# Optimization experiments

Measured on AMD Instinct MI355X. Metric: run time of the kernel, lower is better.

## Reference

```python
import math
import jax, jax.numpy as jnp
import numpy as np

E = 1024   # embed_dim
H = 16     # num_heads
DH = E // H
EPS = 1e-8

def round_ste(x):
    # straight-through round (matches brevitas STE behavior)
    return x + jax.lax.stop_gradient(jnp.round(x) - x)

def _scale(x, qmax):
    # dynamic per-tensor abs-max scale (stand-in for brevitas calibrated scale)
    return jnp.maximum(jnp.max(jnp.abs(x)) / qmax, EPS)

def fq(x, s, qmin, qmax):
    # fake-quantize: quantize to int grid, dequantize back to float
    return jnp.clip(round_ste(x / s), qmin, qmax) * s

def quant_linear(x, W, b):
    # Int8ActPerTensorFloat input, Int8WeightPerTensorFloat (narrow range) weight, Int32Bias
    s_x = _scale(x, 128.0)
    s_w = _scale(W, 127.0)
    xq = fq(x, s_x, -128, 127)
    wq = fq(W, s_w, -127, 127)
    y = xq @ wq.T
    if b is not None:
        s_b = s_x * s_w
        y = y + round_ste(b / s_b) * s_b
    return y

def setup_inputs() -> dict:
    k = jax.random.key(0)
    ks = jax.random.split(k, 7)
    S, B = 1024, 4
    return {
        "query": jax.random.normal(ks[0], (S, B, E), jnp.float32),
        "key": jax.random.normal(ks[1], (S, B, E), jnp.float32),
        "value": jax.random.normal(ks[2], (S, B, E), jnp.float32),
        "in_proj_weight": jax.random.normal(ks[3], (3 * E, E), jnp.float32) * 0.02,
        "in_proj_bias": jax.random.normal(ks[4], (3 * E,), jnp.float32) * 0.02,
        "out_proj_weight": jax.random.normal(ks[5], (E, E), jnp.float32) * 0.02,
        "out_proj_bias": jax.random.normal(ks[6], (E,), jnp.float32) * 0.02,
    }

def reference(query, key, value, in_proj_weight, in_proj_bias, out_proj_weight, out_proj_bias):
    S, B, _ = query.shape
    Wq, Wk, Wv = jnp.split(in_proj_weight, 3, axis=0)
    bq, bk, bv = jnp.split(in_proj_bias, 3)
    # quantized QKV projections (packed in_proj split per-input)
    q = quant_linear(query, Wq, bq)   # (S,B,E)
    k = quant_linear(key, Wk, bk)
    v = quant_linear(value, Wv, bv)

    def to_heads(x):  # (S,B,E) -> (B*H, S, DH)
        return x.reshape(S, B * H, DH).transpose(1, 0, 2)

    q = to_heads(q)
    k = to_heads(k)
    v = to_heads(v)

    # q_scaled quant (int8)
    q = q / math.sqrt(DH)
    q = fq(q, _scale(q, 128.0), -128, 127)
    # k_transposed quant (int8)
    kt = k.transpose(0, 2, 1)  # (B*H, DH, S)
    kt = fq(kt, _scale(kt, 128.0), -128, 127)

    attn = q @ kt                      # (B*H, S, S); softmax_input_quant=None -> identity
    attn = jax.nn.softmax(attn, axis=-1)
    # attn_output_weights quant (uint8)
    s_a = jnp.maximum(jnp.max(attn) / 255.0, EPS)
    attn = jnp.clip(round_ste(attn / s_a), 0, 255) * s_a
    # v quant (int8)
    v = fq(v, _scale(v, 128.0), -128, 127)

    out = attn @ v                     # (B*H, S, DH)
    out = out.transpose(1, 0, 2).reshape(S, B, E)
    out = quant_linear(out, out_proj_weight, out_proj_bias)
    return out
```

## Files before the change

### kernel.cpp

```cpp
#include <hip/hip_runtime.h>
#include <stdint.h>

typedef unsigned short u16;
typedef __attribute__((ext_vector_type(8))) short bf16x8;
typedef __attribute__((ext_vector_type(4))) float f32x4;

#define S_LEN 1024
#define BATCH 4
#define EMB   1024
#define NH    16
#define DHEAD 64
#define BHEAD 64
#define NTOK  4096
#define KDIM  1024
#define NDIM  1024
#define EPSF  1e-8f
#define LOG2E 1.4426950408889634f

#define MFMA16(a,b,c) __builtin_amdgcn_mfma_f32_16x16x32_bf16((a),(b),(c),0,0,0)

#define GLOAD16(g, l) __builtin_amdgcn_global_load_lds( \
    (const __attribute__((address_space(1))) void*)(g), \
    (__attribute__((address_space(3))) void*)(l), 16, 0, 0)

#define EXP2F(x) __builtin_amdgcn_exp2f(x)

__device__ __forceinline__ u16 f2bf(float f){
  return (u16)(__float_as_uint(f) >> 16);
}

__device__ __forceinline__ float wave_max(float v){
#pragma unroll
  for (int off = 32; off > 0; off >>= 1) v = fmaxf(v, __shfl_xor(v, off));
  return v;
}


__global__ void k_zero(float* sc){
  if (threadIdx.x < 16) sc[threadIdx.x] = 0.0f;
}

struct AQDesc { const float* x; u16* y; int n4; int slot; float qdiv; float lo; };
struct AQTable { AQDesc d[7]; };

__global__ __launch_bounds__(256) void k_absmax7(AQTable t, int* __restrict__ sci){
  const int bid = blockIdx.x;
  int seg, b0, nb;
  if (bid < 1536){ seg = bid >> 9; b0 = seg << 9; nb = 512; }
  else { seg = 3 + ((bid - 1536) >> 7); b0 = 1536 + ((seg - 3) << 7); nb = 128; }
  const AQDesc D = t.d[seg];
  float m = 0.0f;
  const float4* x4 = (const float4*)D.x;
  for (int i = (bid - b0)*256 + threadIdx.x; i < D.n4; i += nb*256){
    float4 v = x4[i];
    m = fmaxf(m, fmaxf(fmaxf(fabsf(v.x), fabsf(v.y)), fmaxf(fabsf(v.z), fabsf(v.w))));
  }
  m = wave_max(m);
  __shared__ float red[4];
  int lane = threadIdx.x & 63, w = threadIdx.x >> 6;
  if (lane == 0) red[w] = m;
  __syncthreads();
  if (threadIdx.x == 0){
    float mm = fmaxf(fmaxf(red[0], red[1]), fmaxf(red[2], red[3]));
    atomicMax(sci + D.slot, __float_as_int(mm));
  }
}

__global__ __launch_bounds__(256) void k_quant7(AQTable t, const float* __restrict__ sc){
  const int bid = blockIdx.x;
  int seg, b0, nb;
  if (bid < 1536){ seg = bid >> 9; b0 = seg << 9; nb = 512; }
  else { seg = 3 + ((bid - 1536) >> 7); b0 = 1536 + ((seg - 3) << 7); nb = 128; }
  const AQDesc D = t.d[seg];
  const float s = fmaxf(sc[D.slot] / D.qdiv, EPSF);
  const float lo = D.lo;
  const float4* x4 = (const float4*)D.x;
  for (int i = (bid - b0)*256 + threadIdx.x; i < D.n4; i += nb*256){
    float4 v = x4[i];
    union { u16 o[4]; uint2 u; } ou;
    float tt;
    tt = fminf(fmaxf(rintf(v.x / s), lo), 127.f); ou.o[0] = f2bf(tt);
    tt = fminf(fmaxf(rintf(v.y / s), lo), 127.f); ou.o[1] = f2bf(tt);
    tt = fminf(fmaxf(rintf(v.z / s), lo), 127.f); ou.o[2] = f2bf(tt);
    tt = fminf(fmaxf(rintf(v.w / s), lo), 127.f); ou.o[3] = f2bf(tt);
    ((uint2*)D.y)[i] = ou.u;
  }
}

__global__ __launch_bounds__(256) void k_quant(const float* __restrict__ x,
    u16* __restrict__ y, int n4, const float* __restrict__ sc, int slot){
  const float s = fmaxf(sc[slot] / 128.0f, EPSF);
  const float4* x4 = (const float4*)x;
  for (int i = blockIdx.x*256 + threadIdx.x; i < n4; i += gridDim.x*256){
    float4 v = x4[i];
    union { u16 o[4]; uint2 u; } ou;
    float tt;
    tt = fminf(fmaxf(rintf(v.x / s), -128.f), 127.f); ou.o[0] = f2bf(tt);
    tt = fminf(fmaxf(rintf(v.y / s), -128.f), 127.f); ou.o[1] = f2bf(tt);
    tt = fminf(fmaxf(rintf(v.z / s), -128.f), 127.f); ou.o[2] = f2bf(tt);
    tt = fminf(fmaxf(rintf(v.w / s), -128.f), 127.f); ou.o[3] = f2bf(tt);
    ((uint2*)y)[i] = ou.u;
  }
}

__device__ __forceinline__ void gemm_body(const u16* __restrict__ A,
    const u16* __restrict__ W, const float* __restrict__ bias,
    float* __restrict__ out, float s_b, int rowBase, int colBase,
    int* __restrict__ amax_out, u16 (*As)[64], u16 (*Bs)[64], float* red){
  const int tid = threadIdx.x;
  const int wid = tid >> 6, lane = tid & 63;
  const int wm = wid >> 2, wn = wid & 3;
  const int rr = lane & 15, g = lane >> 4;
  const int srow = wid*8 + (lane >> 3);
  const int sco  = ((lane & 7) ^ (lane >> 3)) << 3;
  const u16* Arow0 = &A[(size_t)(rowBase + srow)*KDIM + sco];
  const u16* Arow1 = &A[(size_t)(rowBase + 64 + srow)*KDIM + sco];
  const u16* Wrow0 = &W[(size_t)(colBase + srow)*KDIM + sco];
  const u16* Wrow1 = &W[(size_t)(colBase + 64 + srow)*KDIM + sco];
  f32x4 c[4][2] = {};
  int aoff[4][2], boff[2][2];
#pragma unroll
  for (int i = 0; i < 4; i++){
    int row = wm*64 + i*16 + rr;
#pragma unroll
    for (int h = 0; h < 2; h++)
      aoff[i][h] = row*64 + (((h*4 + g) ^ (row & 7)) << 3);
  }
#pragma unroll
  for (int j = 0; j < 2; j++){
    int row = wn*32 + j*16 + rr;
#pragma unroll
    for (int h = 0; h < 2; h++)
      boff[j][h] = row*64 + (((h*4 + g) ^ (row & 7)) << 3);
  }
  for (int k0 = 0; k0 < KDIM; k0 += 64){
    __syncthreads();
    GLOAD16(Arow0 + k0, &As[wid*8][0]);
    GLOAD16(Arow1 + k0, &As[64 + wid*8][0]);
    GLOAD16(Wrow0 + k0, &Bs[wid*8][0]);
    GLOAD16(Wrow1 + k0, &Bs[64 + wid*8][0]);
    __syncthreads();
#pragma unroll
    for (int h = 0; h < 2; h++){
      bf16x8 af[4], bfr[2];
#pragma unroll
      for (int i = 0; i < 4; i++) af[i]  = *(const bf16x8*)((const u16*)As + aoff[i][h]);
#pragma unroll
      for (int j = 0; j < 2; j++) bfr[j] = *(const bf16x8*)((const u16*)Bs + boff[j][h]);
#pragma unroll
      for (int i = 0; i < 4; i++)
#pragma unroll
        for (int j = 0; j < 2; j++)
          c[i][j] = MFMA16(af[i], bfr[j], c[i][j]);
    }
  }
  float lmax = 0.0f;
  const int r0 = (lane >> 4) * 4, ccol = lane & 15;
#pragma unroll
  for (int j = 0; j < 2; j++){
    int col = colBase + wn*32 + j*16 + ccol;
    float rb = rintf(bias[col] / s_b);
#pragma unroll
    for (int i = 0; i < 4; i++){
      int rowb = rowBase + wm*64 + i*16 + r0;
#pragma unroll
      for (int rI = 0; rI < 4; rI++){
        float y = s_b * (c[i][j][rI] + rb);
        out[(size_t)(rowb + rI)*NDIM + col] = y;
        lmax = fmaxf(lmax, fabsf(y));
      }
    }
  }
  lmax = wave_max(lmax);
  if (lane == 0) red[wid] = lmax;
  __syncthreads();
  if (tid == 0){
    float mm = red[0];
#pragma unroll
    for (int i2 = 1; i2 < 8; i2++) mm = fmaxf(mm, red[i2]);
    atomicMax(amax_out, __float_as_int(mm));
  }
}

__global__ __launch_bounds__(512) void k_gemm3(const u16* __restrict__ Xall,
    const u16* __restrict__ Wall, const float* __restrict__ ball,
    float* __restrict__ Yall, const float* __restrict__ sc, int* __restrict__ sci){
  __shared__ u16 As[128][64];
  __shared__ u16 Bs[128][64];
  __shared__ float red[8];
  const int orig = blockIdx.x;
  const int xcd = orig & 7, sl = orig >> 3;
  const int seg = sl >> 5;
  const int t2 = xcd*32 + (sl & 31);
  const int by = t2 >> 3, bx = t2 & 7;
  const float s_x = fmaxf(sc[seg] / 128.0f, EPSF);
  const float s_w = fmaxf(sc[3 + seg] / 127.0f, EPSF);
  gemm_body(Xall + (size_t)seg*NTOK*KDIM, Wall + (size_t)seg*KDIM*NDIM,
            ball + seg*1024, Yall + (size_t)seg*NTOK*NDIM, s_x*s_w,
            by*128, bx*128, sci + 7 + seg, As, Bs, red);
}

__global__ __launch_bounds__(512) void k_gemm1(const u16* __restrict__ A,
    const u16* __restrict__ W, const float* __restrict__ bias,
    float* __restrict__ out, const float* __restrict__ sc,
    int sx_slot, int sw_slot, int* __restrict__ amax_out){
  __shared__ u16 As[128][64];
  __shared__ u16 Bs[128][64];
  __shared__ float red[8];
  const int orig = blockIdx.x;
  const int t2 = (orig & 7)*32 + (orig >> 3);
  const int by = t2 >> 3, bx = t2 & 7;
  const float s_x = fmaxf(sc[sx_slot] / 128.0f, EPSF);
  const float s_w = fmaxf(sc[sw_slot] / 127.0f, EPSF);
  gemm_body(A, W, bias, out, s_x*s_w, by*128, bx*128, amax_out, As, Bs, red);
}

__global__ __launch_bounds__(256) void k_quant_heads(const float* __restrict__ qf,
    const float* __restrict__ kf, const float* __restrict__ vf,
    u16* __restrict__ qh, u16* __restrict__ kh, u16* __restrict__ vt,
    const float* __restrict__ sc){
  const float s_q = fmaxf((sc[7]*0.125f)/128.0f, EPSF);
  const float s_k = fmaxf(sc[8]/128.0f, EPSF);
  const float s_v = fmaxf(sc[9]/128.0f, EPSF);
  __shared__ u16 tile[64][80];
  const int bx = blockIdx.x;
  const int st = bx & 15, hh = (bx >> 4) & 15, b = bx >> 8;
  const int t = threadIdx.x;
  const int sl = t >> 2, dc = (t & 3) * 16;
  const size_t row = (size_t)(st*64 + sl)*BATCH + b;
  const size_t ibase = row*EMB + hh*DHEAD + dc;
  const int bh = b*NH + hh;
  float vq[16], vk[16], vv[16];
#pragma unroll
  for (int i = 0; i < 4; i++){
    *(float4*)&vq[i*4] = *(const float4*)&qf[ibase + i*4];
    *(float4*)&vk[i*4] = *(const float4*)&kf[ibase + i*4];
    *(float4*)&vv[i*4] = *(const float4*)&vf[ibase + i*4];
  }
  alignas(16) u16 oq[16], ok[16];
#pragma unroll
  for (int i = 0; i < 16; i++){
    float tq = fminf(fmaxf(rintf((vq[i]*0.125f)/s_q), -128.f), 127.f);
    float tk = fminf(fmaxf(rintf(vk[i]/s_k), -128.f), 127.f);
    float tv = fminf(fmaxf(rintf(vv[i]/s_v), -128.f), 127.f);
    oq[i] = f2bf(tq); ok[i] = f2bf(tk);
    tile[dc + i][sl] = f2bf(tv);
  }
  const size_t qoff = ((size_t)bh*S_LEN + st*64 + sl)*DHEAD + dc;
  *(bf16x8*)&qh[qoff]     = *(const bf16x8*)&oq[0];
  *(bf16x8*)&qh[qoff + 8] = *(const bf16x8*)&oq[8];
  *(bf16x8*)&kh[qoff]     = *(const bf16x8*)&ok[0];
  *(bf16x8*)&kh[qoff + 8] = *(const bf16x8*)&ok[8];
  __syncthreads();
  const int d = t >> 2, sc4 = (t & 3) * 16;
  alignas(16) u16 ov[16];
#pragma unroll
  for (int i = 0; i < 16; i++) ov[i] = tile[d][sc4 + i];
  const size_t voff = ((size_t)bh*DHEAD + d)*S_LEN + st*64 + sc4;
  *(bf16x8*)&vt[voff]     = *(const bf16x8*)&ov[0];
  *(bf16x8*)&vt[voff + 8] = *(const bf16x8*)&ov[8];
}

__global__ __launch_bounds__(256) void k_attn1(const u16* __restrict__ qh,
    const u16* __restrict__ kh, float* __restrict__ mrow, float* __restrict__ lrow,
    const float* __restrict__ sc, int* __restrict__ sci){
  __shared__ u16 Ks[64][64];
  __shared__ float red2[4];
  const int orig = blockIdx.x;
  const int tile = (orig & 7) * 128 + (orig >> 3);
  const int bhead = tile >> 4, q0 = (tile & 15) * 64;
  const int tid = threadIdx.x, w = tid >> 6, lane = tid & 63;
  const int rr = lane & 15, g = lane >> 4, kk = g * 8;
  const int lr3 = lane >> 3, lc = lane & 7;
  const float s_q = fmaxf((sc[7]*0.125f)/128.0f, EPSF);
  const float s_k = fmaxf(sc[8]/128.0f, EPSF);
  const float s_qk = s_q * s_k;
  const u16* qbase = qh + ((size_t)bhead*S_LEN + q0 + w*16)*DHEAD;
  const u16* kbase = kh + (size_t)bhead*S_LEN*DHEAD;
  bf16x8 a0 = *(const bf16x8*)&qbase[rr*DHEAD + kk];
  bf16x8 a1 = *(const bf16x8*)&qbase[rr*DHEAD + 32 + kk];
  float m[4] = {-1e30f, -1e30f, -1e30f, -1e30f};
  float l[4] = {0.f, 0.f, 0.f, 0.f};
  for (int cch = 0; cch < 16; cch++){
    const int n0 = cch * 64;
    __syncthreads();
#pragma unroll
    for (int i = 0; i < 2; i++){
      int r = w*16 + i*8 + lr3;
      GLOAD16(&kbase[(size_t)(n0 + r)*DHEAD + ((lc ^ (r & 7)) << 3)], &Ks[w*16 + i*8][0]);
    }
    __syncthreads();
    float sv[4][4];
#pragma unroll
    for (int nt = 0; nt < 4; nt++){
      int row = nt*16 + rr;
      bf16x8 b0 = *(const bf16x8*)((const u16*)Ks + row*64 + (((g    ) ^ (row & 7)) << 3));
      bf16x8 b1 = *(const bf16x8*)((const u16*)Ks + row*64 + (((4 + g) ^ (row & 7)) << 3));
      f32x4 acc = {};
      acc = MFMA16(a0, b0, acc);
      acc = MFMA16(a1, b1, acc);
#pragma unroll
      for (int r = 0; r < 4; r++) sv[nt][r] = acc[r]*s_qk;
    }
#pragma unroll
    for (int r = 0; r < 4; r++){
      float cm = fmaxf(fmaxf(sv[0][r], sv[1][r]), fmaxf(sv[2][r], sv[3][r]));
      float mn = fmaxf(m[r], cm);
      l[r] *= EXP2F((m[r] - mn)*LOG2E);
      m[r] = mn;
#pragma unroll
      for (int nt = 0; nt < 4; nt++)
        l[r] += EXP2F((sv[nt][r] - m[r])*LOG2E);
    }
  }
#pragma unroll
  for (int off = 1; off < 16; off <<= 1){
#pragma unroll
    for (int r = 0; r < 4; r++){
      float mo = __shfl_xor(m[r], off), lo = __shfl_xor(l[r], off);
      float mn = fmaxf(m[r], mo);
      l[r] = l[r]*EXP2F((m[r] - mn)*LOG2E) + lo*EXP2F((mo - mn)*LOG2E);
      m[r] = mn;
    }
  }
  if (rr == 0){
    int rowb = q0 + w*16 + g*4;
#pragma unroll
    for (int r = 0; r < 4; r++){
      mrow[(size_t)bhead*S_LEN + rowb + r] = m[r];
      lrow[(size_t)bhead*S_LEN + rowb + r] = l[r];
    }
  }
  float im = 0.0f;
#pragma unroll
  for (int r = 0; r < 4; r++) im = fmaxf(im, 1.0f / l[r]);
  im = wave_max(im);
  if (lane == 0) red2[w] = im;
  __syncthreads();
  if (tid == 0){
    float mm = fmaxf(fmaxf(red2[0], red2[1]), fmaxf(red2[2], red2[3]));
    atomicMax(sci + 13, __float_as_int(mm));
  }
}

__global__ void k_sa_final(float* sc, const int* sci){
  if (threadIdx.x == 0)
    sc[11] = fmaxf(__int_as_float(sci[13]) / 255.0f, EPSF);
}

__global__ __launch_bounds__(256) void k_attn2(const u16* __restrict__ qh,
    const u16* __restrict__ kh, const u16* __restrict__ vt,
    const float* __restrict__ mrow, const float* __restrict__ lrow,
    float* __restrict__ aout, const float* __restrict__ sc, int* __restrict__ amax_out){
  __shared__ u16 Ks[64][64];
  __shared__ u16 Vs[64][64];
  __shared__ u16 P[4][16][72];
  __shared__ float red[4];
  const int orig = blockIdx.x;
  const int tile = (orig & 7) * 128 + (orig >> 3);
  const int bhead = tile >> 4, q0 = (tile & 15) * 64;
  const int tid = threadIdx.x, w = tid >> 6, lane = tid & 63;
  const int rr = lane & 15, g = lane >> 4, kk = g * 8;
  const int lr3 = lane >> 3, lc = lane & 7;
  const float s_q = fmaxf((sc[7]*0.125f)/128.0f, EPSF);
  const float s_k = fmaxf(sc[8]/128.0f, EPSF);
  const float s_qk = s_q * s_k;
  const float s_v = fmaxf(sc[9]/128.0f, EPSF);
  const float s_a = sc[11];
  const float fac = s_a * s_v;
  const u16* qbase = qh + ((size_t)bhead*S_LEN + q0 + w*16)*DHEAD;
  const u16* kbase = kh + (size_t)bhead*S_LEN*DHEAD;
  const u16* vbase = vt + (size_t)bhead*DHEAD*S_LEN;
  bf16x8 a0 = *(const bf16x8*)&qbase[rr*DHEAD + kk];
  bf16x8 a1 = *(const bf16x8*)&qbase[rr*DHEAD + 32 + kk];
  float mr[4], inv[4];
  {
    int rowb = q0 + w*16 + g*4;
#pragma unroll
    for (int r = 0; r < 4; r++){
      mr[r]  = mrow[(size_t)bhead*S_LEN + rowb + r];
      inv[r] = 1.0f / (lrow[(size_t)bhead*S_LEN + rowb + r] * s_a);
    }
  }
  f32x4 cpv[4] = {};
  for (int cch = 0; cch < 16; cch++){
    const int n0 = cch * 64;
    __syncthreads();
#pragma unroll
    for (int i = 0; i < 2; i++){
      int r = w*16 + i*8 + lr3;
      GLOAD16(&kbase[(size_t)(n0 + r)*DHEAD + ((lc ^ (r & 7)) << 3)], &Ks[w*16 + i*8][0]);
      int d = w*16 + i*8 + lr3;
      GLOAD16(&vbase[(size_t)d*S_LEN + n0 + ((lc ^ (d & 7)) << 3)], &Vs[w*16 + i*8][0]);
    }
    __syncthreads();
#pragma unroll
    for (int nt = 0; nt < 4; nt++){
      int row = nt*16 + rr;
      bf16x8 b0 = *(const bf16x8*)((const u16*)Ks + row*64 + (((g    ) ^ (row & 7)) << 3));
      bf16x8 b1 = *(const bf16x8*)((const u16*)Ks + row*64 + (((4 + g) ^ (row & 7)) << 3));
      f32x4 acc = {};
      acc = MFMA16(a0, b0, acc);
      acc = MFMA16(a1, b1, acc);
#pragma unroll
      for (int r = 0; r < 4; r++){
        float e  = EXP2F((acc[r]*s_qk - mr[r])*LOG2E);
        float pq = fminf(rintf(e * inv[r]), 255.0f);
        P[w][g*4 + r][nt*16 + rr] = f2bf(pq);
      }
    }
    bf16x8 pa0 = *(const bf16x8*)&P[w][rr][kk];
    bf16x8 pa1 = *(const bf16x8*)&P[w][rr][32 + kk];
#pragma unroll
    for (int f = 0; f < 4; f++){
      int row = f*16 + rr;
      bf16x8 v0 = *(const bf16x8*)((const u16*)Vs + row*64 + (((g    ) ^ (row & 7)) << 3));
      bf16x8 v1 = *(const bf16x8*)((const u16*)Vs + row*64 + (((4 + g) ^ (row & 7)) << 3));
      cpv[f] = MFMA16(pa0, v0, cpv[f]);
      cpv[f] = MFMA16(pa1, v1, cpv[f]);
    }
  }
  const int b = bhead >> 4, hh = bhead & 15;
  float lmax = 0.0f;
#pragma unroll
  for (int f = 0; f < 4; f++){
    int d = f*16 + rr;
#pragma unroll
    for (int r = 0; r < 4; r++){
      int srow = q0 + w*16 + g*4 + r;
      float y = fac * cpv[f][r];
      aout[(size_t)(srow*BATCH + b)*EMB + hh*DHEAD + d] = y;
      lmax = fmaxf(lmax, fabsf(y));
    }
  }
  lmax = wave_max(lmax);
  __syncthreads();
  if (lane == 0) red[w] = lmax;
  __syncthreads();
  if (tid == 0){
    float mm = fmaxf(fmaxf(red[0], red[1]), fmaxf(red[2], red[3]));
    atomicMax(amax_out, __float_as_int(mm));
  }
}

extern "C" void kernel_launch(void* const* d_in, const int* in_sizes, int n_in,
                              void* d_out, int out_size, void* d_ws, size_t ws_size,
                              hipStream_t stream){
  const float* query = (const float*)d_in[0];
  const float* key   = (const float*)d_in[1];
  const float* value = (const float*)d_in[2];
  const float* inW   = (const float*)d_in[3];
  const float* inB   = (const float*)d_in[4];
  const float* outW  = (const float*)d_in[5];
  const float* outB  = (const float*)d_in[6];
  float* out = (float*)d_out;

  char* ws = (char*)d_ws;
  float* sc  = (float*)ws;
  int*   sci = (int*)ws;
  u16* WQQ = (u16*)(ws + 256);
  u16* WKQ = WQQ + 1024*1024;
  u16* WVQ = WKQ + 1024*1024;
  u16* WOQ = WVQ + 1024*1024;
  u16* XQ  = WOQ + 1024*1024;
  u16* XK  = XQ + NTOK*1024;
  u16* XV  = XK + NTOK*1024;
  float* QF = (float*)(XV + NTOK*1024);
  float* KF = QF + NTOK*1024;
  float* VF = KF + NTOK*1024;
  float* MROW = VF + NTOK*1024;
  float* LROW = MROW + BHEAD*S_LEN;
  u16* QH = XQ;  u16* KH = XK;  u16* VT = XV;
  float* AOUT = QF;
  u16* AOQ = (u16*)KF;

  AQTable tab;
  tab.d[0] = { query,             XQ,  NTOK*1024/4, 0, 128.f, -128.f };
  tab.d[1] = { key,               XK,  NTOK*1024/4, 1, 128.f, -128.f };
  tab.d[2] = { value,             XV,  NTOK*1024/4, 2, 128.f, -128.f };
  tab.d[3] = { inW,               WQQ, 1024*1024/4, 3, 127.f, -127.f };
  tab.d[4] = { inW + 1024*1024,   WKQ, 1024*1024/4, 4, 127.f, -127.f };
  tab.d[5] = { inW + 2*1024*1024, WVQ, 1024*1024/4, 5, 127.f, -127.f };
  tab.d[6] = { outW,              WOQ, 1024*1024/4, 6, 127.f, -127.f };

  k_zero<<<1, 64, 0, stream>>>(sc);
  k_absmax7<<<2048, 256, 0, stream>>>(tab, sci);
  k_quant7<<<2048, 256, 0, stream>>>(tab, sc);
  k_gemm3<<<768, 512, 0, stream>>>(XQ, WQQ, inB, QF, sc, sci);
  k_quant_heads<<<1024, 256, 0, stream>>>(QF, KF, VF, QH, KH, VT, sc);
  k_attn1<<<1024, 256, 0, stream>>>(QH, KH, MROW, LROW, sc, sci);
  k_sa_final<<<1, 64, 0, stream>>>(sc, sci);
  k_attn2<<<1024, 256, 0, stream>>>(QH, KH, VT, MROW, LROW, AOUT, sc, sci + 10);
  k_quant<<<1024, 256, 0, stream>>>(AOUT, AOQ, NTOK*1024/4, sc, 10);
  k_gemm1<<<256, 512, 0, stream>>>(AOQ, WOQ, outB, out, sc, 10, 6, sci + 12);
}
```

Before: 213.5 us.

## Switch quantized GEMMs and QK^T to int8 MFMA with int8 storage

Quantized activations and weights are now stored as packed int8 rather than bf16. The projection GEMMs and the QK^T products use the i32 16x16x64 int8 MFMA, which halves operand bytes moved through global memory and LDS and halves the MFMA count per K step. LDS tiles, swizzles and the K-loop step are re-laid out for byte data, and the workspace layout is adjusted so VT gets its own buffer. The PV product stays in bf16, and results are exact because the quantized values are small integers.

```diff
diff --git a/kernel.cpp b/kernel.cpp
--- a/kernel.cpp
+++ b/kernel.cpp
@@ -2,8 +2,11 @@
 #include <stdint.h>
 
 typedef unsigned short u16;
+typedef signed char i8;
+typedef unsigned char u8;
 typedef __attribute__((ext_vector_type(8))) short bf16x8;
 typedef __attribute__((ext_vector_type(4))) float f32x4;
+typedef __attribute__((ext_vector_type(4))) int i32x4;
 
 #define S_LEN 1024
 #define BATCH 4
@@ -17,7 +20,8 @@
 #define EPSF  1e-8f
 #define LOG2E 1.4426950408889634f
 
-#define MFMA16(a,b,c) __builtin_amdgcn_mfma_f32_16x16x32_bf16((a),(b),(c),0,0,0)
+#define MFMA16(a,b,c)  __builtin_amdgcn_mfma_f32_16x16x32_bf16((a),(b),(c),0,0,0)
+#define MFMAI8(a,b,c)  __builtin_amdgcn_mfma_i32_16x16x64_i8((a),(b),(c),0,0,0)
 
 #define GLOAD16(g, l) __builtin_amdgcn_global_load_lds( \
     (const __attribute__((address_space(1))) void*)(g), \
@@ -29,6 +33,12 @@
   return (u16)(__float_as_uint(f) >> 16);
 }
 
+__device__ __forceinline__ unsigned pack4(float a, float b, float c, float d){
+  int qa = (int)a, qb = (int)b, qc = (int)c, qd = (int)d;
+  return (unsigned)(qa & 255) | ((unsigned)(qb & 255) << 8) |
+         ((unsigned)(qc & 255) << 16) | ((unsigned)(qd & 255) << 24);
+}
+
 __device__ __forceinline__ float wave_max(float v){
 #pragma unroll
   for (int off = 32; off > 0; off >>= 1) v = fmaxf(v, __shfl_xor(v, off));
@@ -40,7 +50,7 @@
   if (threadIdx.x < 16) sc[threadIdx.x] = 0.0f;
 }
 
-struct AQDesc { const float* x; u16* y; int n4; int slot; float qdiv; float lo; };
+struct AQDesc { const float* x; u8* y; int n4; int slot; float qdiv; float lo; };
 struct AQTable { AQDesc d[7]; };
 
 __global__ __launch_bounds__(256) void k_absmax7(AQTable t, int* __restrict__ sci){
@@ -75,65 +85,63 @@
   const float s = fmaxf(sc[D.slot] / D.qdiv, EPSF);
   const float lo = D.lo;
   const float4* x4 = (const float4*)D.x;
+  unsigned* y4 = (unsigned*)D.y;
   for (int i = (bid - b0)*256 + threadIdx.x; i < D.n4; i += nb*256){
     float4 v = x4[i];
-    union { u16 o[4]; uint2 u; } ou;
-    float tt;
-    tt = fminf(fmaxf(rintf(v.x / s), lo), 127.f); ou.o[0] = f2bf(tt);
-    tt = fminf(fmaxf(rintf(v.y / s), lo), 127.f); ou.o[1] = f2bf(tt);
-    tt = fminf(fmaxf(rintf(v.z / s), lo), 127.f); ou.o[2] = f2bf(tt);
-    tt = fminf(fmaxf(rintf(v.w / s), lo), 127.f); ou.o[3] = f2bf(tt);
-    ((uint2*)D.y)[i] = ou.u;
+    float t0 = fminf(fmaxf(rintf(v.x / s), lo), 127.f);
+    float t1 = fminf(fmaxf(rintf(v.y / s), lo), 127.f);
+    float t2 = fminf(fmaxf(rintf(v.z / s), lo), 127.f);
+    float t3 = fminf(fmaxf(rintf(v.w / s), lo), 127.f);
+    y4[i] = pack4(t0, t1, t2, t3);
   }
 }
 
 __global__ __launch_bounds__(256) void k_quant(const float* __restrict__ x,
-    u16* __restrict__ y, int n4, const float* __restrict__ sc, int slot){
+    u8* __restrict__ y, int n4, const float* __restrict__ sc, int slot){
   const float s = fmaxf(sc[slot] / 128.0f, EPSF);
   const float4* x4 = (const float4*)x;
+  unsigned* y4 = (unsigned*)y;
   for (int i = blockIdx.x*256 + threadIdx.x; i < n4; i += gridDim.x*256){
     float4 v = x4[i];
-    union { u16 o[4]; uint2 u; } ou;
-    float tt;
-    tt = fminf(fmaxf(rintf(v.x / s), -128.f), 127.f); ou.o[0] = f2bf(tt);
-    tt = fminf(fmaxf(rintf(v.y / s), -128.f), 127.f); ou.o[1] = f2bf(tt);
-    tt = fminf(fmaxf(rintf(v.z / s), -128.f), 127.f); ou.o[2] = f2bf(tt);
-    tt = fminf(fmaxf(rintf(v.w / s), -128.f), 127.f); ou.o[3] = f2bf(tt);
-    ((uint2*)y)[i] = ou.u;
-  }
-}
-
-__device__ __forceinline__ void gemm_body(const u16* __restrict__ A,
-    const u16* __restrict__ W, const float* __restrict__ bias,
+    float t0 = fminf(fmaxf(rintf(v.x / s), -128.f), 127.f);
+    float t1 = fminf(fmaxf(rintf(v.y / s), -128.f), 127.f);
+    float t2 = fminf(fmaxf(rintf(v.z / s), -128.f), 127.f);
+    float t3 = fminf(fmaxf(rintf(v.w / s), -128.f), 127.f);
+    y4[i] = pack4(t0, t1, t2, t3);
+  }
+}
+
+__device__ __forceinline__ void gemm_body(const i8* __restrict__ A,
+    const i8* __restrict__ W, const float* __restrict__ bias,
     float* __restrict__ out, float s_b, int rowBase, int colBase,
-    int* __restrict__ amax_out, u16 (*As)[64], u16 (*Bs)[64], float* red){
+    int* __restrict__ amax_out, i8 (*As)[128], i8 (*Bs)[128], float* red){
   const int tid = threadIdx.x;
   const int wid = tid >> 6, lane = tid & 63;
   const int wm = wid >> 2, wn = wid & 3;
   const int rr = lane & 15, g = lane >> 4;
   const int srow = wid*8 + (lane >> 3);
-  const int sco  = ((lane & 7) ^ (lane >> 3)) << 3;
-  const u16* Arow0 = &A[(size_t)(rowBase + srow)*KDIM + sco];
-  const u16* Arow1 = &A[(size_t)(rowBase + 64 + srow)*KDIM + sco];
-  const u16* Wrow0 = &W[(size_t)(colBase + srow)*KDIM + sco];
-  const u16* Wrow1 = &W[(size_t)(colBase + 64 + srow)*KDIM + sco];
-  f32x4 c[4][2] = {};
+  const int sco  = ((lane & 7) ^ (lane >> 3)) << 4;
+  const i8* Arow0 = &A[(size_t)(rowBase + srow)*KDIM + sco];
+  const i8* Arow1 = &A[(size_t)(rowBase + 64 + srow)*KDIM + sco];
+  const i8* Wrow0 = &W[(size_t)(colBase + srow)*KDIM + sco];
+  const i8* Wrow1 = &W[(size_t)(colBase + 64 + srow)*KDIM + sco];
+  i32x4 c[4][2] = {};
   int aoff[4][2], boff[2][2];
 #pragma unroll
   for (int i = 0; i < 4; i++){
     int row = wm*64 + i*16 + rr;
 #pragma unroll
     for (int h = 0; h < 2; h++)
-      aoff[i][h] = row*64 + (((h*4 + g) ^ (row & 7)) << 3);
+      aoff[i][h] = row*128 + (((h*4 + g) ^ (row & 7)) << 4);
   }
 #pragma unroll
   for (int j = 0; j < 2; j++){
     int row = wn*32 + j*16 + rr;
 #pragma unroll
     for (int h = 0; h < 2; h++)
-      boff[j][h] = row*64 + (((h*4 + g) ^ (row & 7)) << 3);
-  }
-  for (int k0 = 0; k0 < KDIM; k0 += 64){
+      boff[j][h] = row*128 + (((h*4 + g) ^ (row & 7)) << 4);
+  }
+  for (int k0 = 0; k0 < KDIM; k0 += 128){
     __syncthreads();
     GLOAD16(Arow0 + k0, &As[wid*8][0]);
     GLOAD16(Arow1 + k0, &As[64 + wid*8][0]);
@@ -142,16 +150,16 @@
     __syncthreads();
 #pragma unroll
     for (int h = 0; h < 2; h++){
-      bf16x8 af[4], bfr[2];
-#pragma unroll
-      for (int i = 0; i < 4; i++) af[i]  = *(const bf16x8*)((const u16*)As + aoff[i][h]);
-#pragma unroll
-      for (int j = 0; j < 2; j++) bfr[j] = *(const bf16x8*)((const u16*)Bs + boff[j][h]);
+      i32x4 af[4], bfr[2];
+#pragma unroll
+      for (int i = 0; i < 4; i++) af[i]  = *(const i32x4*)((const i8*)As + aoff[i][h]);
+#pragma unroll
+      for (int j = 0; j < 2; j++) bfr[j] = *(const i32x4*)((const i8*)Bs + boff[j][h]);
 #pragma unroll
       for (int i = 0; i < 4; i++)
 #pragma unroll
         for (int j = 0; j < 2; j++)
-          c[i][j] = MFMA16(af[i], bfr[j], c[i][j]);
+          c[i][j] = MFMAI8(af[i], bfr[j], c[i][j]);
     }
   }
   float lmax = 0.0f;
@@ -165,7 +173,7 @@
       int rowb = rowBase + wm*64 + i*16 + r0;
 #pragma unroll
       for (int rI = 0; rI < 4; rI++){
-        float y = s_b * (c[i][j][rI] + rb);
+        float y = s_b * ((float)c[i][j][rI] + rb);
         out[(size_t)(rowb + rI)*NDIM + col] = y;
         lmax = fmaxf(lmax, fabsf(y));
       }
@@ -182,11 +190,11 @@
   }
 }
 
-__global__ __launch_bounds__(512) void k_gemm3(const u16* __restrict__ Xall,
-    const u16* __restrict__ Wall, const float* __restrict__ ball,
+__global__ __launch_bounds__(512) void k_gemm3(const i8* __restrict__ Xall,
+    const i8* __restrict__ Wall, const float* __restrict__ ball,
     float* __restrict__ Yall, const float* __restrict__ sc, int* __restrict__ sci){
-  __shared__ u16 As[128][64];
-  __shared__ u16 Bs[128][64];
+  __shared__ i8 As[128][128];
+  __shared__ i8 Bs[128][128];
   __shared__ float red[8];
   const int orig = blockIdx.x;
   const int xcd = orig & 7, sl = orig >> 3;
@@ -200,12 +208,12 @@
             by*128, bx*128, sci + 7 + seg, As, Bs, red);
 }
 
-__global__ __launch_bounds__(512) void k_gemm1(const u16* __restrict__ A,
-    const u16* __restrict__ W, const float* __restrict__ bias,
+__global__ __launch_bounds__(512) void k_gemm1(const i8* __restrict__ A,
+    const i8* __restrict__ W, const float* __restrict__ bias,
     float* __restrict__ out, const float* __restrict__ sc,
     int sx_slot, int sw_slot, int* __restrict__ amax_out){
-  __shared__ u16 As[128][64];
-  __shared__ u16 Bs[128][64];
+  __shared__ i8 As[128][128];
+  __shared__ i8 Bs[128][128];
   __shared__ float red[8];
   const int orig = blockIdx.x;
   const int t2 = (orig & 7)*32 + (orig >> 3);
@@ -217,7 +225,7 @@
 
 __global__ __launch_bounds__(256) void k_quant_heads(const float* __restrict__ qf,
     const float* __restrict__ kf, const float* __restrict__ vf,
-    u16* __restrict__ qh, u16* __restrict__ kh, u16* __restrict__ vt,
+    i8* __restrict__ qh, i8* __restrict__ kh, u16* __restrict__ vt,
     const float* __restrict__ sc){
   const float s_q = fmaxf((sc[7]*0.125f)/128.0f, EPSF);
   const float s_k = fmaxf(sc[8]/128.0f, EPSF);
@@ -237,20 +245,18 @@
     *(float4*)&vk[i*4] = *(const float4*)&kf[ibase + i*4];
     *(float4*)&vv[i*4] = *(const float4*)&vf[ibase + i*4];
   }
-  alignas(16) u16 oq[16], ok[16];
+  alignas(16) i8 oq[16], ok[16];
 #pragma unroll
   for (int i = 0; i < 16; i++){
     float tq = fminf(fmaxf(rintf((vq[i]*0.125f)/s_q), -128.f), 127.f);
     float tk = fminf(fmaxf(rintf(vk[i]/s_k), -128.f), 127.f);
     float tv = fminf(fmaxf(rintf(vv[i]/s_v), -128.f), 127.f);
-    oq[i] = f2bf(tq); ok[i] = f2bf(tk);
+    oq[i] = (i8)(int)tq; ok[i] = (i8)(int)tk;
     tile[dc + i][sl] = f2bf(tv);
   }
   const size_t qoff = ((size_t)bh*S_LEN + st*64 + sl)*DHEAD + dc;
-  *(bf16x8*)&qh[qoff]     = *(const bf16x8*)&oq[0];
-  *(bf16x8*)&qh[qoff + 8] = *(const bf16x8*)&oq[8];
-  *(bf16x8*)&kh[qoff]     = *(const bf16x8*)&ok[0];
-  *(bf16x8*)&kh[qoff + 8] = *(const bf16x8*)&ok[8];
+  *(int4*)&qh[qoff] = *(const int4*)&oq[0];
+  *(int4*)&kh[qoff] = *(const int4*)&ok[0];
   __syncthreads();
   const int d = t >> 2, sc4 = (t & 3) * 16;
   alignas(16) u16 ov[16];
@@ -261,46 +267,40 @@
   *(bf16x8*)&vt[voff + 8] = *(const bf16x8*)&ov[8];
 }
 
-__global__ __launch_bounds__(256) void k_attn1(const u16* __restrict__ qh,
-    const u16* __restrict__ kh, float* __restrict__ mrow, float* __restrict__ lrow,
+__global__ __launch_bounds__(256) void k_attn1(const i8* __restrict__ qh,
+    const i8* __restrict__ kh, float* __restrict__ mrow, float* __restrict__ lrow,
     const float* __restrict__ sc, int* __restrict__ sci){
-  __shared__ u16 Ks[64][64];
+  __shared__ i8 Ks[64][64];
   __shared__ float red2[4];
   const int orig = blockIdx.x;
   const int tile = (orig & 7) * 128 + (orig >> 3);
   const int bhead = tile >> 4, q0 = (tile & 15) * 64;
   const int tid = threadIdx.x, w = tid >> 6, lane = tid & 63;
-  const int rr = lane & 15, g = lane >> 4, kk = g * 8;
-  const int lr3 = lane >> 3, lc = lane & 7;
+  const int rr = lane & 15, g = lane >> 4;
   const float s_q = fmaxf((sc[7]*0.125f)/128.0f, EPSF);
   const float s_k = fmaxf(sc[8]/128.0f, EPSF);
   const float s_qk = s_q * s_k;
-  const u16* qbase = qh + ((size_t)bhead*S_LEN + q0 + w*16)*DHEAD;
-  const u16* kbase = kh + (size_t)bhead*S_LEN*DHEAD;
-  bf16x8 a0 = *(const bf16x8*)&qbase[rr*DHEAD + kk];
-  bf16x8 a1 = *(const bf16x8*)&qbase[rr*DHEAD + 32 + kk];
+  const i8* qbase = qh + ((size_t)bhead*S_LEN + q0 + w*16)*DHEAD;
+  const i8* kbase = kh + (size_t)bhead*S_LEN*DHEAD;
+  i32x4 a = *(const i32x4*)&qbase[rr*DHEAD + g*16];
+  const int srow = w*16 + (lane >> 2);
+  const int sco  = ((lane & 3) ^ ((srow >> 1) & 3)) << 4;
   float m[4] = {-1e30f, -1e30f, -1e30f, -1e30f};
   float l[4] = {0.f, 0.f, 0.f, 0.f};
   for (int cch = 0; cch < 16; cch++){
     const int n0 = cch * 64;
     __syncthreads();
-#pragma unroll
-    for (int i = 0; i < 2; i++){
-      int r = w*16 + i*8 + lr3;
-      GLOAD16(&kbase[(size_t)(n0 + r)*DHEAD + ((lc ^ (r & 7)) << 3)], &Ks[w*16 + i*8][0]);
-    }
+    GLOAD16(&kbase[(size_t)(n0 + srow)*DHEAD + sco], &Ks[w*16][0]);
     __syncthreads();
     float sv[4][4];
 #pragma unroll
     for (int nt = 0; nt < 4; nt++){
       int row = nt*16 + rr;
-      bf16x8 b0 = *(const bf16x8*)((const u16*)Ks + row*64 + (((g    ) ^ (row & 7)) << 3));
-      bf16x8 b1 = *(const bf16x8*)((const u16*)Ks + row*64 + (((4 + g) ^ (row & 7)) << 3));
-      f32x4 acc = {};
-      acc = MFMA16(a0, b0, acc);
-      acc = MFMA16(a1, b1, acc);
-#pragma unroll
-      for (int r = 0; r < 4; r++) sv[nt][r] = acc[r]*s_qk;
+      i32x4 b = *(const i32x4*)((const i8*)Ks + row*64 + (((g ^ ((row >> 1) & 3))) << 4));
+      i32x4 acc = {};
+      acc = MFMAI8(a, b, acc);
+#pragma unroll
+      for (int r = 0; r < 4; r++) sv[nt][r] = (float)acc[r]*s_qk;
     }
 #pragma unroll
     for (int r = 0; r < 4; r++){
@@ -348,11 +348,11 @@
     sc[11] = fmaxf(__int_as_float(sci[13]) / 255.0f, EPSF);
 }
 
-__global__ __launch_bounds__(256) void k_attn2(const u16* __restrict__ qh,
-    const u16* __restrict__ kh, const u16* __restrict__ vt,
+__global__ __launch_bounds__(256) void k_attn2(const i8* __restrict__ qh,
+    const i8* __restrict__ kh, const u16* __restrict__ vt,
     const float* __restrict__ mrow, const float* __restrict__ lrow,
     float* __restrict__ aout, const float* __restrict__ sc, int* __restrict__ amax_out){
-  __shared__ u16 Ks[64][64];
+  __shared__ i8 Ks[64][64];
   __shared__ u16 Vs[64][64];
   __shared__ u16 P[4][16][72];
   __shared__ float red[4];
@@ -368,11 +368,10 @@
   const float s_v = fmaxf(sc[9]/128.0f, EPSF);
   const float s_a = sc[11];
   const float fac = s_a * s_v;
-  const u16* qbase = qh + ((size_t)bhead*S_LEN + q0 + w*16)*DHEAD;
-  const u16* kbase = kh + (size_t)bhead*S_LEN*DHEAD;
+  const i8* qbase = qh + ((size_t)bhead*S_LEN + q0 + w*16)*DHEAD;
+  const i8* kbase = kh + (size_t)bhead*S_LEN*DHEAD;
   const u16* vbase = vt + (size_t)bhead*DHEAD*S_LEN;
-  bf16x8 a0 = *(const bf16x8*)&qbase[rr*DHEAD + kk];
-  bf16x8 a1 = *(const bf16x8*)&qbase[rr*DHEAD + 32 + kk];
+  i32x4 a = *(const i32x4*)&qbase[rr*DHEAD + g*16];
   float mr[4], inv[4];
   {
     int rowb = q0 + w*16 + g*4;
@@ -382,14 +381,15 @@
       inv[r] = 1.0f / (lrow[(size_t)bhead*S_LEN + rowb + r] * s_a);
     }
   }
+  const int srow = w*16 + (lane >> 2);
+  const int sco  = ((lane & 3) ^ ((srow >> 1) & 3)) << 4;
   f32x4 cpv[4] = {};
   for (int cch = 0; cch < 16; cch++){
     const int n0 = cch * 64;
     __syncthreads();
+    GLOAD16(&kbase[(size_t)(n0 + srow)*DHEAD + sco], &Ks[w*16][0]);
 #pragma unroll
     for (int i = 0; i < 2; i++){
-      int r = w*16 + i*8 + lr3;
-      GLOAD16(&kbase[(size_t)(n0 + r)*DHEAD + ((lc ^ (r & 7)) << 3)], &Ks[w*16 + i*8][0]);
       int d = w*16 + i*8 + lr3;
       GLOAD16(&vbase[(size_t)d*S_LEN + n0 + ((lc ^ (d & 7)) << 3)], &Vs[w*16 + i*8][0]);
     }
@@ -397,14 +397,12 @@
 #pragma unroll
     for (int nt = 0; nt < 4; nt++){
       int row = nt*16 + rr;
-      bf16x8 b0 = *(const bf16x8*)((const u16*)Ks + row*64 + (((g    ) ^ (row & 7)) << 3));
-      bf16x8 b1 = *(const bf16x8*)((const u16*)Ks + row*64 + (((4 + g) ^ (row & 7)) << 3));
-      f32x4 acc = {};
-      acc = MFMA16(a0, b0, acc);
-      acc = MFMA16(a1, b1, acc);
+      i32x4 b = *(const i32x4*)((const i8*)Ks + row*64 + (((g ^ ((row >> 1) & 3))) << 4));
+      i32x4 acc = {};
+      acc = MFMAI8(a, b, acc);
 #pragma unroll
       for (int r = 0; r < 4; r++){
-        float e  = EXP2F((acc[r]*s_qk - mr[r])*LOG2E);
+        float e  = EXP2F(((float)acc[r]*s_qk - mr[r])*LOG2E);
         float pq = fminf(rintf(e * inv[r]), 255.0f);
         P[w][g*4 + r][nt*16 + rr] = f2bf(pq);
       }
@@ -427,9 +425,9 @@
     int d = f*16 + rr;
 #pragma unroll
     for (int r = 0; r < 4; r++){
-      int srow = q0 + w*16 + g*4 + r;
+      int srow2 = q0 + w*16 + g*4 + r;
       float y = fac * cpv[f][r];
-      aout[(size_t)(srow*BATCH + b)*EMB + hh*DHEAD + d] = y;
+      aout[(size_t)(srow2*BATCH + b)*EMB + hh*DHEAD + d] = y;
       lmax = fmaxf(lmax, fabsf(y));
     }
   }
@@ -458,21 +456,22 @@
   char* ws = (char*)d_ws;
   float* sc  = (float*)ws;
   int*   sci = (int*)ws;
-  u16* WQQ = (u16*)(ws + 256);
-  u16* WKQ = WQQ + 1024*1024;
-  u16* WVQ = WKQ + 1024*1024;
-  u16* WOQ = WVQ + 1024*1024;
-  u16* XQ  = WOQ + 1024*1024;
-  u16* XK  = XQ + NTOK*1024;
-  u16* XV  = XK + NTOK*1024;
-  float* QF = (float*)(XV + NTOK*1024);
-  float* KF = QF + NTOK*1024;
-  float* VF = KF + NTOK*1024;
-  float* MROW = VF + NTOK*1024;
+  u8* WQQ = (u8*)(ws + 256);
+  u8* WKQ = WQQ + 1024*1024;
+  u8* WVQ = WKQ + 1024*1024;
+  u8* WOQ = WVQ + 1024*1024;
+  u8* XQ  = WOQ + 1024*1024;
+  u8* XK  = XQ + (size_t)NTOK*1024;
+  u8* XV  = XK + (size_t)NTOK*1024;
+  float* QF = (float*)(XV + (size_t)NTOK*1024);
+  float* KF = QF + (size_t)NTOK*1024;
+  float* VF = KF + (size_t)NTOK*1024;
+  u16* VT = (u16*)(VF + (size_t)NTOK*1024);
+  float* MROW = (float*)(VT + (size_t)BHEAD*DHEAD*S_LEN);
   float* LROW = MROW + BHEAD*S_LEN;
-  u16* QH = XQ;  u16* KH = XK;  u16* VT = XV;
+  i8* QH  = (i8*)XQ;   i8* KH = (i8*)XK;
   float* AOUT = QF;
-  u16* AOQ = (u16*)KF;
+  u8* AOQ = XV;
 
   AQTable tab;
   tab.d[0] = { query,             XQ,  NTOK*1024/4, 0, 128.f, -128.f };
@@ -486,11 +485,11 @@
   k_zero<<<1, 64, 0, stream>>>(sc);
   k_absmax7<<<2048, 256, 0, stream>>>(tab, sci);
   k_quant7<<<2048, 256, 0, stream>>>(tab, sc);
-  k_gemm3<<<768, 512, 0, stream>>>(XQ, WQQ, inB, QF, sc, sci);
+  k_gemm3<<<768, 512, 0, stream>>>((const i8*)XQ, (const i8*)WQQ, inB, QF, sc, sci);
   k_quant_heads<<<1024, 256, 0, stream>>>(QF, KF, VF, QH, KH, VT, sc);
   k_attn1<<<1024, 256, 0, stream>>>(QH, KH, MROW, LROW, sc, sci);
   k_sa_final<<<1, 64, 0, stream>>>(sc, sci);
   k_attn2<<<1024, 256, 0, stream>>>(QH, KH, VT, MROW, LROW, AOUT, sc, sci + 10);
   k_quant<<<1024, 256, 0, stream>>>(AOUT, AOQ, NTOK*1024/4, sc, 10);
-  k_gemm1<<<256, 512, 0, stream>>>(AOQ, WOQ, outB, out, sc, 10, 6, sci + 12);
-}
+  k_gemm1<<<256, 512, 0, stream>>>((const i8*)AOQ, (const i8*)WOQ, outB, out, sc, 10, 6, sci + 12);
+}
```

New measurement: 187.7 us. 1.14x faster.
